# Kernel optimization log

Hardware: AMD Instinct MI355X
Metric: run time of the kernel (lower is better)

## Reference

```python
import jax, jax.numpy as jnp
import numpy as np

TOPK = 13
ALPHA = 1.0
BETA = 6.0
EPS = 1e-9


def _make_boxes(key, lead_shape, img=640.0):
    kc, ks = jax.random.split(key)
    c = jax.random.uniform(kc, lead_shape + (2,), minval=0.0, maxval=img)
    s = jax.random.uniform(ks, lead_shape + (2,), minval=16.0, maxval=160.0)
    return jnp.concatenate([c - s * 0.5, c + s * 0.5], axis=-1)


def setup_inputs() -> dict:
    key = jax.random.key(0)
    ks = jax.random.split(key, 8)
    B, L, C, N, K = 32, 8400, 1, 64, 17
    pred_scores = jax.random.uniform(ks[0], (B, L, C), dtype=jnp.float32)
    pred_bboxes = _make_boxes(ks[1], (B, L))
    pred_poses = jax.random.normal(ks[2], (B, L, K, 3), dtype=jnp.float32)
    anchor_points = jax.random.uniform(ks[3], (L, 2), minval=0.0, maxval=640.0)
    gt_labels = jax.random.randint(ks[4], (B, N, 1), 0, C)
    gt_bboxes = _make_boxes(ks[5], (B, N))
    gt_poses = jax.random.normal(ks[6], (B, N, K, 3), dtype=jnp.float32)
    counts = jax.random.randint(ks[7], (B,), 8, N + 1)
    pad_gt_mask = (jnp.arange(N)[None, :] < counts[:, None]).astype(jnp.float32)[..., None]
    return dict(pred_scores=pred_scores, pred_bboxes=pred_bboxes, pred_poses=pred_poses,
                anchor_points=anchor_points, gt_labels=gt_labels, gt_bboxes=gt_bboxes,
                gt_poses=gt_poses, pad_gt_mask=pad_gt_mask, bg_index=C)


def _batch_iou(box1, box2, eps=EPS):
    # box1: [B,n,4], box2: [B,L,4] -> [B,n,L]
    a = box1[:, :, None, :]
    b = box2[:, None, :, :]
    lt = jnp.maximum(a[..., :2], b[..., :2])
    rb = jnp.minimum(a[..., 2:], b[..., 2:])
    wh = jnp.clip(rb - lt, 0.0)
    inter = wh[..., 0] * wh[..., 1]
    area_a = (a[..., 2] - a[..., 0]) * (a[..., 3] - a[..., 1])
    area_b = (b[..., 2] - b[..., 0]) * (b[..., 3] - b[..., 1])
    return inter / (area_a + area_b - inter + eps)


def _points_in_boxes(points, bboxes, eps=EPS):
    # points: [L,2], bboxes: [B,n,4] -> [B,n,L] float
    x, y = points[:, 0], points[:, 1]
    x1 = bboxes[..., 0:1]; y1 = bboxes[..., 1:2]
    x2 = bboxes[..., 2:3]; y2 = bboxes[..., 3:4]
    m = jnp.minimum(jnp.minimum(x - x1, y - y1), jnp.minimum(x2 - x, y2 - y))
    return (m > eps).astype(bboxes.dtype)


def _gather_topk_anchors(metrics, topk, topk_mask):
    # metrics: [B,n,L]; topk_mask: [B,n,1]
    B, n, L = metrics.shape
    _, idxs = jax.lax.top_k(metrics, topk)  # [B,n,K]
    is_in_topk = jnp.zeros_like(metrics).at[
        jnp.arange(B)[:, None, None], jnp.arange(n)[None, :, None], idxs].add(1.0)
    return is_in_topk * topk_mask


def _compute_max_iou_anchor(ious):
    # ious: [B,n,L] -> one-hot over gt dim of argmax gt per anchor
    n = ious.shape[-2]
    idx = jnp.argmax(ious, axis=-2)  # [B,L]
    return (jnp.arange(n)[None, :, None] == idx[:, None, :]).astype(ious.dtype)


def reference(pred_scores, pred_bboxes, pred_poses, anchor_points, gt_labels,
              gt_bboxes, gt_poses, pad_gt_mask, bg_index):
    B, L, C = pred_scores.shape
    n = gt_bboxes.shape[1]
    K = pred_poses.shape[2]

    ious = _batch_iou(gt_bboxes, pred_bboxes)  # [B,n,L]
    scores_t = jnp.transpose(pred_scores, (0, 2, 1))  # [B,C,L]
    bbox_cls_scores = scores_t[jnp.arange(B)[:, None], gt_labels[..., 0]]  # [B,n,L]
    alignment_metrics = (bbox_cls_scores ** ALPHA) * (ious ** BETA)

    is_in_gts = _points_in_boxes(anchor_points, gt_bboxes)  # [B,n,L]
    is_in_topk = _gather_topk_anchors(alignment_metrics * is_in_gts, TOPK, pad_gt_mask)
    mask_positive = is_in_topk * is_in_gts * pad_gt_mask  # [B,n,L]
    mask_positive_sum = mask_positive.sum(axis=-2)  # [B,L]

    # resolve anchors assigned to multiple gts by max IoU (no-op when no conflicts)
    mask_multiple_gts = jnp.broadcast_to((mask_positive_sum[:, None, :] > 1), mask_positive.shape)
    is_max_iou = _compute_max_iou_anchor(ious)
    mask_positive = jnp.where(mask_multiple_gts, is_max_iou, mask_positive)
    mask_positive_sum = mask_positive.sum(axis=-2)

    assigned_gt_index = jnp.argmax(mask_positive, axis=-2)  # [B,L]
    assigned_gt_index = assigned_gt_index + jnp.arange(B)[:, None] * n  # flat offset
    flat = assigned_gt_index.reshape(-1)

    assigned_labels = jnp.take(gt_labels.reshape(-1), flat).reshape(B, L)
    assigned_labels = jnp.where(mask_positive_sum > 0, assigned_labels,
                                jnp.full_like(assigned_labels, bg_index))
    assigned_bboxes = gt_bboxes.reshape(-1, 4)[flat].reshape(B, L, 4)
    assigned_poses = gt_poses.reshape(-1, K, 3)[flat].reshape(B, L, K, 3)

    one_hot = jax.nn.one_hot(assigned_labels, C + 1, dtype=pred_scores.dtype)
    keep = np.array([i for i in range(C + 1) if i != bg_index])
    assigned_scores = one_hot[..., keep]  # [B,L,C]

    am = alignment_metrics * mask_positive
    max_metrics = am.max(axis=-1, keepdims=True)  # [B,n,1]
    max_ious = (ious * mask_positive).max(axis=-1, keepdims=True)
    am = am / (max_metrics + EPS) * max_ious
    am = am.max(axis=-2)[..., None]  # [B,L,1]
    assigned_scores = assigned_scores * am

    return assigned_labels, assigned_bboxes, assigned_poses, assigned_scores, assigned_gt_index
```

## Files before the change

### kernel.cpp

```cpp
#include <hip/hip_runtime.h>
#include <hip/hip_bf16.h>

#define BB    32
#define LL    8400
#define NGT   64
#define CCH   1
#define KPT   17
#define NTOPK 13
#define POOL  2048

#define OFF_LAB  ((size_t)0)
#define OFF_BOX  ((size_t)268800)
#define OFF_POSE ((size_t)1344000)
#define OFF_SC   ((size_t)15052800)
#define OFF_GI   ((size_t)15321600)


__device__ __forceinline__ float iou_pair(float gx1, float gy1, float gx2, float gy2,
                                          float px1, float py1, float px2, float py2)
{
#pragma clang fp contract(off)
    float ltx = fmaxf(gx1, px1);
    float lty = fmaxf(gy1, py1);
    float rbx = fminf(gx2, px2);
    float rby = fminf(gy2, py2);
    float w = fmaxf(rbx - ltx, 0.0f);
    float h = fmaxf(rby - lty, 0.0f);
    float inter = w * h;
    float ag = (gx2 - gx1) * (gy2 - gy1);
    float ap = (px2 - px1) * (py2 - py1);
    return inter / (ag + ap - inter + 1e-9f);
}

__device__ __forceinline__ bool in_box(float ax, float ay,
                                       float gx1, float gy1, float gx2, float gy2)
{
#pragma clang fp contract(off)
    float m = fminf(fminf(ax - gx1, ay - gy1), fminf(gx2 - ax, gy2 - ay));
    return m > 1e-9f;
}

__device__ __forceinline__ float pow6(float x)
{
#pragma clang fp contract(off)
    float x2 = x * x;
    return (x2 * x2) * x2;
}


__global__ __launch_bounds__(256) void topk_kernel(
    const float* __restrict__ pred_scores,
    const float* __restrict__ pred_bboxes,
    const float* __restrict__ anchor_points,
    const int*   __restrict__ gt_labels,
    const float* __restrict__ gt_bboxes,
    const float* __restrict__ pad_gt_mask,
    unsigned*    __restrict__ cells)
{
    __shared__ unsigned long long pool[POOL];
    __shared__ unsigned long long wlists[4 * NTOPK];
    __shared__ int cnt;

    int b = blockIdx.x >> 6;
    int i = blockIdx.x & 63;
    if (pad_gt_mask[b * NGT + i] == 0.0f) return;

    int tid = threadIdx.x;
    if (tid == 0) cnt = 0;
    __syncthreads();

    int gbase = (b * NGT + i) * 4;
    float gx1 = gt_bboxes[gbase + 0];
    float gy1 = gt_bboxes[gbase + 1];
    float gx2 = gt_bboxes[gbase + 2];
    float gy2 = gt_bboxes[gbase + 3];
    int lbl = gt_labels[b * NGT + i];

    int lane = tid & 63;
    int wave = tid >> 6;

#pragma unroll 4
    for (int l = tid; l < LL; l += 256) {
        int pidx = b * LL + l;
        float4 pb = reinterpret_cast<const float4*>(pred_bboxes)[pidx];
        float iou = iou_pair(gx1, gy1, gx2, gy2, pb.x, pb.y, pb.z, pb.w);
        float score = pred_scores[pidx * CCH + lbl];
        float metric = score * pow6(iou);
        float2 ap = reinterpret_cast<const float2*>(anchor_points)[l];
        float v = in_box(ap.x, ap.y, gx1, gy1, gx2, gy2) ? metric : 0.0f;

        if ((v > 0.0f) || (l < 2 * NTOPK)) {
            int slot = atomicAdd(&cnt, 1);
            if (slot < POOL) {
                unsigned long long key =
                    ((unsigned long long)__float_as_uint(v) << 32) |
                    (unsigned long long)(0xFFFFFFFFu - (unsigned)l);
                pool[slot] = key;
            }
        }
    }
    __syncthreads();

    int total = cnt;
    if (total <= POOL) {
#pragma unroll
        for (int k = 0; k < NTOPK; ++k) {
            unsigned long long lm = 0;
            int li = -1;
            for (int e = wave * 64 + lane; e < total; e += 256) {
                unsigned long long pv = pool[e];
                if (pv > lm) { lm = pv; li = e; }
            }
            unsigned long long m = lm;
#pragma unroll
            for (int off = 32; off > 0; off >>= 1) {
                unsigned long long o = __shfl_xor(m, off);
                m = o > m ? o : m;
            }
            if (lane == 0) wlists[wave * NTOPK + k] = m;
            if (li >= 0 && lm == m) pool[li] = 0;
        }
    } else {
        unsigned long long prev = ~0ull;
        for (int k = 0; k < NTOPK; ++k) {
            unsigned long long lm = 0;
            for (int l = wave * 64 + lane; l < LL; l += 256) {
                int pidx = b * LL + l;
                float4 pb = reinterpret_cast<const float4*>(pred_bboxes)[pidx];
                float iou = iou_pair(gx1, gy1, gx2, gy2, pb.x, pb.y, pb.z, pb.w);
                float score = pred_scores[pidx * CCH + lbl];
                float metric = score * pow6(iou);
                float2 ap = reinterpret_cast<const float2*>(anchor_points)[l];
                float v = in_box(ap.x, ap.y, gx1, gy1, gx2, gy2) ? metric : 0.0f;
                unsigned long long key =
                    ((unsigned long long)__float_as_uint(v) << 32) |
                    (unsigned long long)(0xFFFFFFFFu - (unsigned)l);
                if (key < prev && key > lm) lm = key;
            }
            unsigned long long m = lm;
#pragma unroll
            for (int off = 32; off > 0; off >>= 1) {
                unsigned long long o = __shfl_xor(m, off);
                m = o > m ? o : m;
            }
            if (lane == 0) wlists[wave * NTOPK + k] = m;
            prev = m;
        }
    }
    __syncthreads();

    if (tid == 0) {
        int p0 = 0, p1 = 0, p2 = 0, p3 = 0;
        for (int k = 0; k < NTOPK; ++k) {
            unsigned long long k0 = wlists[0 * NTOPK + p0];
            unsigned long long k1 = wlists[1 * NTOPK + p1];
            unsigned long long k2 = wlists[2 * NTOPK + p2];
            unsigned long long k3 = wlists[3 * NTOPK + p3];
            unsigned long long m01 = k0 >= k1 ? k0 : k1;
            unsigned long long m23 = k2 >= k3 ? k2 : k3;
            unsigned long long m = m01 >= m23 ? m01 : m23;
            if (m == k0)      ++p0;
            else if (m == k1) ++p1;
            else if (m == k2) ++p2;
            else              ++p3;
            if (m == 0ull) continue;

            unsigned lw = 0xFFFFFFFFu - (unsigned)(m & 0xFFFFFFFFull);
            float v = __uint_as_float((unsigned)(m >> 32));
            bool posw;
            if (v > 0.0f) {
                posw = true;
            } else {
                float2 ap = reinterpret_cast<const float2*>(anchor_points)[lw];
                posw = in_box(ap.x, ap.y, gx1, gy1, gx2, gy2);
            }
            if (posw)
                atomicAdd(&cells[b * LL + lw], 1u + ((unsigned)i << 8));
        }
    }
}


__global__ __launch_bounds__(256) void decode_kernel(
    const float* __restrict__ pred_scores,
    const float* __restrict__ pred_bboxes,
    const int*   __restrict__ gt_labels,
    const float* __restrict__ gt_bboxes,
    const unsigned* __restrict__ cells,
    int*      __restrict__ assigned,
    unsigned* __restrict__ rowmax_metric,
    unsigned* __restrict__ rowmax_iou)
{
    __shared__ float gsh[NGT * 4];
    int b = blockIdx.y;
    int tid = threadIdx.x;
    for (int k = tid; k < NGT * 4; k += 256) gsh[k] = gt_bboxes[b * NGT * 4 + k];
    __syncthreads();

    int l = blockIdx.x * 256 + tid;
    if (l >= LL) return;
    int idx = b * LL + l;

    unsigned cell = cells[idx];
    int cnt = (int)(cell & 0xFFu);
    if (cnt == 0) { assigned[idx] = -1; return; }

    float px1 = pred_bboxes[idx * 4 + 0];
    float py1 = pred_bboxes[idx * 4 + 1];
    float px2 = pred_bboxes[idx * 4 + 2];
    float py2 = pred_bboxes[idx * 4 + 3];

    int istar;
    if (cnt == 1) {
        int v = (int)(cell >> 8);
        istar = (v >= 0 && v < NGT) ? v : 0;
    } else {
        float best = -1.0f;
        int bi = 0;
        for (int i = 0; i < NGT; ++i) {
            float iou = iou_pair(gsh[i * 4 + 0], gsh[i * 4 + 1], gsh[i * 4 + 2], gsh[i * 4 + 3],
                                 px1, py1, px2, py2);
            if (iou > best) { best = iou; bi = i; }
        }
        istar = bi;
    }
    assigned[idx] = istar;

    float iou = iou_pair(gsh[istar * 4 + 0], gsh[istar * 4 + 1], gsh[istar * 4 + 2], gsh[istar * 4 + 3],
                         px1, py1, px2, py2);
    int lbl = gt_labels[b * NGT + istar];
    float score = pred_scores[idx * CCH + lbl];
    float met = score * pow6(iou);
    atomicMax(&rowmax_metric[b * NGT + istar], __float_as_uint(met));
    atomicMax(&rowmax_iou[b * NGT + istar], __float_as_uint(iou));
}


__global__ __launch_bounds__(256) void write_kernel(
    const float* __restrict__ pred_scores,
    const float* __restrict__ pred_bboxes,
    const int*   __restrict__ gt_labels,
    const float* __restrict__ gt_bboxes,
    const int*      __restrict__ assigned,
    const unsigned* __restrict__ rowmax_metric,
    const unsigned* __restrict__ rowmax_iou,
    const int*   __restrict__ bg_ptr,
    float* __restrict__ out)
{
    __shared__ float gsh[NGT * 4];
    int b = blockIdx.y;
    int tid = threadIdx.x;
    for (int k = tid; k < NGT * 4; k += 256) gsh[k] = gt_bboxes[b * NGT * 4 + k];
    __syncthreads();

    int l = blockIdx.x * 256 + tid;
    if (l >= LL) return;
    int idx = b * LL + l;

    int a = assigned[idx];
    bool pos = a >= 0;
    int agi = pos ? a : 0;
    int bg = *bg_ptr;
    int lbl = pos ? gt_labels[b * NGT + agi] : bg;

    out[OFF_LAB + (size_t)idx] = (float)lbl;
    out[OFF_GI + (size_t)idx]  = (float)(b * NGT + agi);

    float4 box;
    box.x = gsh[agi * 4 + 0];
    box.y = gsh[agi * 4 + 1];
    box.z = gsh[agi * 4 + 2];
    box.w = gsh[agi * 4 + 3];
    reinterpret_cast<float4*>(out + OFF_BOX)[idx] = box;

    float am = 0.0f;
    if (pos) {
        float px1 = pred_bboxes[idx * 4 + 0];
        float py1 = pred_bboxes[idx * 4 + 1];
        float px2 = pred_bboxes[idx * 4 + 2];
        float py2 = pred_bboxes[idx * 4 + 3];
        float iou = iou_pair(box.x, box.y, box.z, box.w, px1, py1, px2, py2);
        float score = pred_scores[idx * CCH + gt_labels[b * NGT + a]];
        float met = score * pow6(iou);
        float mm = __uint_as_float(rowmax_metric[b * NGT + a]);
        float mi = __uint_as_float(rowmax_iou[b * NGT + a]);
        am = met / (mm + 1e-9f) * mi;
    }
    int kc = (bg == 0) ? 1 : 0;
    out[OFF_SC + (size_t)idx] = (lbl == kc) ? am : 0.0f;
}


__global__ __launch_bounds__(256) void pose_kernel(
    const float* __restrict__ gt_poses,
    const int*   __restrict__ assigned,
    float* __restrict__ out_poses)
{
    const int TOT = BB * LL * KPT * 3;
    int e = blockIdx.x * 256 + threadIdx.x;
    if (e >= TOT) return;
    int anchor = e / (KPT * 3);
    int j = e - anchor * (KPT * 3);
    int b = anchor / LL;
    int a = assigned[anchor];
    int agi = a >= 0 ? a : 0;
    out_poses[e] = gt_poses[(size_t)(b * NGT + agi) * (KPT * 3) + j];
}


extern "C" void kernel_launch(void* const* d_in, const int* in_sizes, int n_in,
                              void* d_out, int out_size, void* d_ws, size_t ws_size,
                              hipStream_t stream)
{
    const float* pred_scores   = (const float*)d_in[0];
    const float* pred_bboxes   = (const float*)d_in[1];
    const float* anchor_points = (const float*)d_in[3];
    const int*   gt_labels     = (const int*)d_in[4];
    const float* gt_bboxes     = (const float*)d_in[5];
    const float* gt_poses      = (const float*)d_in[6];
    const float* pad_gt_mask   = (const float*)d_in[7];
    const int*   bg_ptr        = (const int*)d_in[8];

    char* ws = (char*)d_ws;
    unsigned* cells         = (unsigned*)ws;
    unsigned* rowmax_metric = (unsigned*)(ws + 1075200);
    unsigned* rowmax_iou    = (unsigned*)(ws + 1083392);
    int*      assigned      = (int*)(ws + 1091584);

    hipMemsetAsync(d_ws, 0, 1091584, stream);

    topk_kernel<<<BB * NGT, 256, 0, stream>>>(
        pred_scores, pred_bboxes, anchor_points, gt_labels, gt_bboxes, pad_gt_mask, cells);

    dim3 gridBL((LL + 255) / 256, BB);
    decode_kernel<<<gridBL, 256, 0, stream>>>(
        pred_scores, pred_bboxes, gt_labels, gt_bboxes, cells,
        assigned, rowmax_metric, rowmax_iou);

    write_kernel<<<gridBL, 256, 0, stream>>>(
        pred_scores, pred_bboxes, gt_labels, gt_bboxes,
        assigned, rowmax_metric, rowmax_iou, bg_ptr, (float*)d_out);

    const int TOT = BB * LL * KPT * 3;
    pose_kernel<<<(TOT + 255) / 256, 256, 0, stream>>>(
        gt_poses, assigned, (float*)d_out + OFF_POSE);
}
```

Before: 95.63 us.

## Bin anchors into a spatial grid so top-k scans only anchors inside each GT box

Adds a single-block kernel that buckets the 8400 anchor points into a 32x32 grid of 20-pixel cells, sorted by bin with a prefix-sum index. The top-k kernel then visits only the bins overlapping each GT box, instead of computing IoU and metric for every anchor per GT, and seeds the pool with zero-valued fallbacks for the first 26 anchors. The pose gather kernel now writes float4s, four outputs per thread. The cost is one extra serial single-block launch, and the sparse pool fill has to match the old zero-padding tie-break semantics.

```diff
diff --git a/kernel.cpp b/kernel.cpp
--- a/kernel.cpp
+++ b/kernel.cpp
@@ -8,6 +8,7 @@
 #define KPT   17
 #define NTOPK 13
 #define POOL  2048
+#define NBIN  32
 
 #define OFF_LAB  ((size_t)0)
 #define OFF_BOX  ((size_t)268800)
@@ -47,6 +48,57 @@
     return (x2 * x2) * x2;
 }
 
+__device__ __forceinline__ int bin_of(float x)
+{
+    int v = (int)floorf(x * 0.05f);
+    return v < 0 ? 0 : (v > NBIN - 1 ? NBIN - 1 : v);
+}
+
+
+__global__ __launch_bounds__(1024) void build_bins_kernel(
+    const float* __restrict__ anchor_points,
+    int*   __restrict__ bin_start,
+    int*   __restrict__ bin_id,
+    float2* __restrict__ bin_xy)
+{
+    __shared__ int c[NBIN * NBIN];
+    __shared__ int off[NBIN * NBIN];
+    int tid = threadIdx.x;
+
+    c[tid] = 0;
+    __syncthreads();
+    for (int l = tid; l < LL; l += 1024) {
+        float2 ap = reinterpret_cast<const float2*>(anchor_points)[l];
+        int bin = bin_of(ap.y) * NBIN + bin_of(ap.x);
+        atomicAdd(&c[bin], 1);
+    }
+    __syncthreads();
+
+    off[tid] = c[tid];
+    __syncthreads();
+    for (int s = 1; s < NBIN * NBIN; s <<= 1) {
+        int v = (tid >= s) ? off[tid - s] : 0;
+        __syncthreads();
+        off[tid] += v;
+        __syncthreads();
+    }
+    bin_start[tid + 1] = off[tid];
+    if (tid == 0) bin_start[0] = 0;
+    c[tid] = 0;
+    __syncthreads();
+
+    int base = (tid == 0) ? 0 : off[tid - 1];
+    (void)base;
+    for (int l = tid; l < LL; l += 1024) {
+        float2 ap = reinterpret_cast<const float2*>(anchor_points)[l];
+        int bin = bin_of(ap.y) * NBIN + bin_of(ap.x);
+        int st = (bin == 0) ? 0 : off[bin - 1];
+        int slot = st + atomicAdd(&c[bin], 1);
+        bin_id[slot] = l;
+        bin_xy[slot] = ap;
+    }
+}
+
 
 __global__ __launch_bounds__(256) void topk_kernel(
     const float* __restrict__ pred_scores,
@@ -55,6 +107,9 @@
     const int*   __restrict__ gt_labels,
     const float* __restrict__ gt_bboxes,
     const float* __restrict__ pad_gt_mask,
+    const int*   __restrict__ bin_start,
+    const int*   __restrict__ bin_id,
+    const float2* __restrict__ bin_xy,
     unsigned*    __restrict__ cells)
 {
     __shared__ unsigned long long pool[POOL];
@@ -79,23 +134,34 @@
     int lane = tid & 63;
     int wave = tid >> 6;
 
-#pragma unroll 4
-    for (int l = tid; l < LL; l += 256) {
-        int pidx = b * LL + l;
-        float4 pb = reinterpret_cast<const float4*>(pred_bboxes)[pidx];
-        float iou = iou_pair(gx1, gy1, gx2, gy2, pb.x, pb.y, pb.z, pb.w);
-        float score = pred_scores[pidx * CCH + lbl];
-        float metric = score * pow6(iou);
-        float2 ap = reinterpret_cast<const float2*>(anchor_points)[l];
-        float v = in_box(ap.x, ap.y, gx1, gy1, gx2, gy2) ? metric : 0.0f;
-
-        if ((v > 0.0f) || (l < 2 * NTOPK)) {
+    if (tid < 2 * NTOPK) {
+        float2 ap = reinterpret_cast<const float2*>(anchor_points)[tid];
+        if (!in_box(ap.x, ap.y, gx1, gy1, gx2, gy2)) {
             int slot = atomicAdd(&cnt, 1);
-            if (slot < POOL) {
-                unsigned long long key =
-                    ((unsigned long long)__float_as_uint(v) << 32) |
-                    (unsigned long long)(0xFFFFFFFFu - (unsigned)l);
-                pool[slot] = key;
+            pool[slot] = (unsigned long long)(0xFFFFFFFFu - (unsigned)tid);
+        }
+    }
+
+    int bx0 = bin_of(gx1), bx1 = bin_of(gx2);
+    int by0 = bin_of(gy1), by1 = bin_of(gy2);
+    for (int by = by0; by <= by1; ++by) {
+        int s = bin_start[by * NBIN + bx0];
+        int e = bin_start[by * NBIN + bx1 + 1];
+        for (int t = s + tid; t < e; t += 256) {
+            float2 ap = bin_xy[t];
+            if (in_box(ap.x, ap.y, gx1, gy1, gx2, gy2)) {
+                int l = bin_id[t];
+                int pidx = b * LL + l;
+                float4 pb = reinterpret_cast<const float4*>(pred_bboxes)[pidx];
+                float iou = iou_pair(gx1, gy1, gx2, gy2, pb.x, pb.y, pb.z, pb.w);
+                float score = pred_scores[pidx * CCH + lbl];
+                float v = score * pow6(iou);
+                int slot = atomicAdd(&cnt, 1);
+                if (slot < POOL) {
+                    pool[slot] =
+                        ((unsigned long long)__float_as_uint(v) << 32) |
+                        (unsigned long long)(0xFFFFFFFFu - (unsigned)l);
+                }
             }
         }
     }
@@ -296,15 +362,24 @@
     const int*   __restrict__ assigned,
     float* __restrict__ out_poses)
 {
-    const int TOT = BB * LL * KPT * 3;
-    int e = blockIdx.x * 256 + threadIdx.x;
-    if (e >= TOT) return;
-    int anchor = e / (KPT * 3);
-    int j = e - anchor * (KPT * 3);
-    int b = anchor / LL;
-    int a = assigned[anchor];
-    int agi = a >= 0 ? a : 0;
-    out_poses[e] = gt_poses[(size_t)(b * NGT + agi) * (KPT * 3) + j];
+    const int TOT4 = BB * LL * KPT * 3 / 4;
+    int c = blockIdx.x * 256 + threadIdx.x;
+    if (c >= TOT4) return;
+    int e0 = c * 4;
+    float r[4];
+#pragma unroll
+    for (int u = 0; u < 4; ++u) {
+        int e = e0 + u;
+        int anchor = e / (KPT * 3);
+        int j = e - anchor * (KPT * 3);
+        int b = anchor / LL;
+        int a = assigned[anchor];
+        int agi = a >= 0 ? a : 0;
+        r[u] = gt_poses[(size_t)(b * NGT + agi) * (KPT * 3) + j];
+    }
+    float4 v;
+    v.x = r[0]; v.y = r[1]; v.z = r[2]; v.w = r[3];
+    reinterpret_cast<float4*>(out_poses)[c] = v;
 }
 
 
@@ -326,11 +401,17 @@
     unsigned* rowmax_metric = (unsigned*)(ws + 1075200);
     unsigned* rowmax_iou    = (unsigned*)(ws + 1083392);
     int*      assigned      = (int*)(ws + 1091584);
+    int*      bin_start     = (int*)(ws + 2166784);
+    int*      bin_id        = (int*)(ws + 2170888);
+    float2*   bin_xy        = (float2*)(ws + 2204488);
 
     hipMemsetAsync(d_ws, 0, 1091584, stream);
 
+    build_bins_kernel<<<1, 1024, 0, stream>>>(anchor_points, bin_start, bin_id, bin_xy);
+
     topk_kernel<<<BB * NGT, 256, 0, stream>>>(
-        pred_scores, pred_bboxes, anchor_points, gt_labels, gt_bboxes, pad_gt_mask, cells);
+        pred_scores, pred_bboxes, anchor_points, gt_labels, gt_bboxes, pad_gt_mask,
+        bin_start, bin_id, bin_xy, cells);
 
     dim3 gridBL((LL + 255) / 256, BB);
     decode_kernel<<<gridBL, 256, 0, stream>>>(
@@ -341,7 +422,7 @@
         pred_scores, pred_bboxes, gt_labels, gt_bboxes,
         assigned, rowmax_metric, rowmax_iou, bg_ptr, (float*)d_out);
 
-    const int TOT = BB * LL * KPT * 3;
-    pose_kernel<<<(TOT + 255) / 256, 256, 0, stream>>>(
+    const int TOT4 = BB * LL * KPT * 3 / 4;
+    pose_kernel<<<(TOT4 + 255) / 256, 256, 0, stream>>>(
         gt_poses, assigned, (float*)d_out + OFF_POSE);
 }
```

Measured after the change: 96.12 us. No clear change (+0.5%).
